# Kernel tuning notes

Hardware: AMD Instinct MI355X
Metric: run time of the kernel (lower is better)

## Reference

```python
import jax, jax.numpy as jnp
import numpy as np

N_USER, N_FOOD, N_ING, N_CAT, N_HAB = 50000, 50000, 50000, 5000, 5000
N_NODES = N_USER + N_FOOD + N_ING + N_CAT + N_HAB  # 160000
E = 600000
R = 8
D = 128  # common_dim == hidden_dim


def _linear(x, W, b):
    # W: (in, out)
    return x @ W + b


def _rgcn_conv(x, src, dst, edge_type, W, root, bias):
    """PyG RGCNConv with aggr='mean': out = x@root + bias + sum_r mean_{r-edges into i}(W_r x_j)."""
    n = x.shape[0]
    out = x @ root + bias
    for r in range(R):  # static small loop over relations
        mask = (edge_type == r)
        h_r = x @ W[r]                          # (N, O)
        msg = h_r[src] * mask[:, None].astype(x.dtype)  # (E, O)
        s = jax.ops.segment_sum(msg, dst, num_segments=n)
        cnt = jax.ops.segment_sum(mask.astype(x.dtype), dst, num_segments=n)
        out = out + s / jnp.maximum(cnt, 1.0)[:, None]
    return out


def setup_inputs() -> dict:
    key = jax.random.key(0)
    ks = jax.random.split(key, 32)
    s = 0.05
    inp = {
        'x_user': jax.random.normal(ks[0], (N_USER, 256), jnp.float32),
        'x_food': jax.random.normal(ks[1], (N_FOOD, 128), jnp.float32),
        'x_ingredient': jax.random.normal(ks[2], (N_ING, 128), jnp.float32),
        'x_category': jax.random.normal(ks[3], (N_CAT, 64), jnp.float32),
        'x_habit': jax.random.normal(ks[4], (N_HAB, 64), jnp.float32),
        'edge_index': jax.random.randint(ks[5], (2, E), 0, N_NODES, jnp.int32),
        'edge_type': jax.random.randint(ks[6], (E,), 0, R, jnp.int32),
        # init linears (in, out)
        'Wu': jax.random.normal(ks[7], (256, D), jnp.float32) * s,
        'bu': jnp.zeros((D,), jnp.float32),
        'Wf': jax.random.normal(ks[8], (128, D), jnp.float32) * s,
        'bf': jnp.zeros((D,), jnp.float32),
        'Wi': jax.random.normal(ks[9], (128, D), jnp.float32) * s,
        'bi': jnp.zeros((D,), jnp.float32),
        'Wc': jax.random.normal(ks[10], (64, D), jnp.float32) * s,
        'bc': jnp.zeros((D,), jnp.float32),
        'Wh': jax.random.normal(ks[11], (64, D), jnp.float32) * s,
        'bh': jnp.zeros((D,), jnp.float32),
        # conv1
        'W1': jax.random.normal(ks[12], (R, D, D), jnp.float32) * s,
        'root1': jax.random.normal(ks[13], (D, D), jnp.float32) * s,
        'bias1': jnp.zeros((D,), jnp.float32),
        # conv2
        'W2': jax.random.normal(ks[14], (R, D, D), jnp.float32) * s,
        'root2': jax.random.normal(ks[15], (D, D), jnp.float32) * s,
        'bias2': jnp.zeros((D,), jnp.float32),
    }
    return inp


def reference(x_user, x_food, x_ingredient, x_category, x_habit,
              edge_index, edge_type,
              Wu, bu, Wf, bf, Wi, bi, Wc, bc, Wh, bh,
              W1, root1, bias1, W2, root2, bias2):
    # per-type input projections then concat in fixed order
    x_all = jnp.concatenate([
        _linear(x_user, Wu, bu),
        _linear(x_food, Wf, bf),
        _linear(x_ingredient, Wi, bi),
        _linear(x_category, Wc, bc),
        _linear(x_habit, Wh, bh),
    ], axis=0)  # (N_NODES, D)
    src, dst = edge_index[0], edge_index[1]
    x = _rgcn_conv(x_all, src, dst, edge_type, W1, root1, bias1)
    x = jax.nn.relu(x)
    # dropout is identity in eval mode
    x = _rgcn_conv(x, src, dst, edge_type, W2, root2, bias2)
    return x
```

## Files before the change

### kernel.cpp

```cpp
#include <hip/hip_runtime.h>

typedef unsigned short ushort_t;
typedef unsigned int uint_t;
typedef __attribute__((ext_vector_type(8))) __bf16 bf16x8;
typedef __attribute__((ext_vector_type(4))) float f32x4;
typedef __attribute__((ext_vector_type(4))) uint_t uint4v;

#define NN 160000
#define DD 128
#define EE 600000
#define RR 8
#define NRR (NN * RR)
#define WTOT 376832

__device__ __forceinline__ ushort_t f2b(float f) {
  uint_t u = __float_as_uint(f);
  u = u + 0x7fffu + ((u >> 16) & 1u);
  return (ushort_t)(u >> 16);
}
__device__ __forceinline__ float b2f(ushort_t u) {
  return __uint_as_float(((uint_t)u) << 16);
}

__device__ __forceinline__ void gload_lds16(const ushort_t* g, ushort_t* l) {
  __builtin_amdgcn_global_load_lds(
      (const __attribute__((address_space(1))) void*)g,
      (__attribute__((address_space(3))) void*)l, 16, 0, 0);
}

struct WSrcs { const float* s[9]; };

__global__ void wconv_all_kernel(WSrcs srcs, ushort_t* __restrict__ wbuf) {
  int i = blockIdx.x * blockDim.x + threadIdx.x;
  if (i >= WTOT) return;
  int m, start, K;
  if      (i < 32768)  { m = 0; start = 0;      K = 256; }
  else if (i < 49152)  { m = 1; start = 32768;  K = 128; }
  else if (i < 65536)  { m = 2; start = 49152;  K = 128; }
  else if (i < 73728)  { m = 3; start = 65536;  K = 64;  }
  else if (i < 81920)  { m = 4; start = 73728;  K = 64;  }
  else if (i < 98304)  { m = 5; start = 81920;  K = 128; }
  else if (i < 114688) { m = 6; start = 98304;  K = 128; }
  else if (i < 245760) { m = 7; start = 114688; K = 128; }
  else                 { m = 8; start = 245760; K = 128; }
  int local = i - start;
  int per = K * 128;
  int mat = local / per, rem = local - mat * per;
  int k = rem >> 7, n = rem & 127;
  ushort_t v = f2b(srcs.s[m][local]);
  if (m < 5) {
    wbuf[start + mat * per + n * K + k] = v;
  } else {
    int kc = k >> 3, kr = k & 7;
    int slot = kc ^ (n & 7);
    wbuf[start + mat * per + n * 128 + slot * 8 + kr] = v;
  }
}

__global__ __launch_bounds__(256, 2) void gemm_proj(
    const float* __restrict__ Ain, const ushort_t* __restrict__ WT,
    const float* __restrict__ bias, ushort_t* __restrict__ Cout, int M, int K) {
  __shared__ ushort_t As[128 * 128];
  __shared__ ushort_t Ws[128 * 128];
  const int tid = threadIdx.x;
  const int bm = blockIdx.x * 128;
  const int wave = tid >> 6, lane = tid & 63;
  const int lr = lane & 15;
  const int lg = lane >> 4;

  f32x4 acc[2][8];
#pragma unroll
  for (int mt = 0; mt < 2; ++mt)
#pragma unroll
    for (int nt = 0; nt < 8; ++nt) acc[mt][nt] = {0.f, 0.f, 0.f, 0.f};

  for (int k0 = 0; k0 < K; k0 += 128) {
#pragma unroll
    for (int it = 0; it < 8; ++it) {
      int row = it * 16 + (tid >> 4);
      int c = tid & 15;
      uint4v val = {0, 0, 0, 0};
      int grow = bm + row, gk = k0 + c * 8;
      if (grow < M && gk < K) {
        const float* ap = Ain + (size_t)grow * K + gk;
        float4 v0 = *(const float4*)ap;
        float4 v1 = *(const float4*)(ap + 4);
        val[0] = (uint_t)f2b(v0.x) | ((uint_t)f2b(v0.y) << 16);
        val[1] = (uint_t)f2b(v0.z) | ((uint_t)f2b(v0.w) << 16);
        val[2] = (uint_t)f2b(v1.x) | ((uint_t)f2b(v1.y) << 16);
        val[3] = (uint_t)f2b(v1.z) | ((uint_t)f2b(v1.w) << 16);
      }
      *(uint4v*)&As[row * 128 + ((c ^ (row & 7)) * 8)] = val;
    }
#pragma unroll
    for (int it = 0; it < 8; ++it) {
      int n = it * 16 + (tid >> 4);
      int c = tid & 15;
      uint4v val = {0, 0, 0, 0};
      int gk = k0 + c * 8;
      if (gk < K)
        val = *(const uint4v*)(WT + (size_t)n * K + gk);
      *(uint4v*)&Ws[n * 128 + ((c ^ (n & 7)) * 8)] = val;
    }
    __syncthreads();
#pragma unroll
    for (int ks = 0; ks < 4; ++ks) {
      int chunk = ks * 4 + lg;
      bf16x8 af[2], bfr[8];
#pragma unroll
      for (int mt = 0; mt < 2; ++mt) {
        int row = wave * 32 + mt * 16 + lr;
        af[mt] = *(const bf16x8*)&As[row * 128 + ((chunk ^ (row & 7)) * 8)];
      }
#pragma unroll
      for (int nt = 0; nt < 8; ++nt) {
        int n = nt * 16 + lr;
        bfr[nt] = *(const bf16x8*)&Ws[n * 128 + ((chunk ^ (n & 7)) * 8)];
      }
#pragma unroll
      for (int mt = 0; mt < 2; ++mt)
#pragma unroll
        for (int nt = 0; nt < 8; ++nt)
          acc[mt][nt] = __builtin_amdgcn_mfma_f32_16x16x32_bf16(
              af[mt], bfr[nt], acc[mt][nt], 0, 0, 0);
    }
    __syncthreads();
  }

  float bv[8];
#pragma unroll
  for (int nt = 0; nt < 8; ++nt) bv[nt] = bias[nt * 16 + lr];

#pragma unroll
  for (int mt = 0; mt < 2; ++mt) {
    int rbase = bm + wave * 32 + mt * 16 + lg * 4;
#pragma unroll
    for (int i = 0; i < 4; ++i) {
      int row = rbase + i;
      if (row >= M) continue;
#pragma unroll
      for (int nt = 0; nt < 8; ++nt)
        Cout[(size_t)row * 128 + nt * 16 + lr] = f2b(acc[mt][nt][i] + bv[nt]);
    }
  }
}

template <bool RELU_BF>
__global__ __launch_bounds__(512, 4) void rgcn_conv(
    const ushort_t* __restrict__ xin, const int* __restrict__ seg_off,
    const int* __restrict__ sorted_src,
    const ushort_t* __restrict__ WrT,
    const ushort_t* __restrict__ rootT,
    const float* __restrict__ bias,
    float* __restrict__ fout, ushort_t* __restrict__ bfout) {
  __shared__ ushort_t As[64 * 128];
  __shared__ ushort_t Ws[128 * 128];
  const int tid = threadIdx.x;
  const int bm = blockIdx.x * 64;
  const int wave = tid >> 6, lane = tid & 63;
  const int wm = wave & 3;
  const int wn = wave >> 2;
  const int lr = lane & 15, lg = lane >> 4;
  const int grp = tid >> 4;
  const int sl = tid & 15;

  f32x4 acc[4];
#pragma unroll
  for (int nt = 0; nt < 4; ++nt) acc[nt] = {0.f, 0.f, 0.f, 0.f};

  int gsv[8][2], gev[8][2];
  int s0v[8][2], s1v[8][2];
  uint4v f0v[8][2], f1v[8][2];
  uint4v rootv[2];

#define BOUNDS(P)                                                         \
  {                                                                       \
    _Pragma("unroll") for (int q = 0; q < 2; ++q) {                       \
      int g = (P) * NN + bm + q * 32 + grp;                               \
      gsv[P][q] = seg_off[g];                                             \
      gev[P][q] = seg_off[g + 1];                                         \
    }                                                                     \
  }

#define SRCS(P)                                                           \
  {                                                                       \
    _Pragma("unroll") for (int q = 0; q < 2; ++q) {                       \
      int a = gsv[P][q];                                                  \
      int c = gev[P][q] - a;                                              \
      int i0 = (a < EE - 1) ? a : (EE - 1);                               \
      int i1 = (c > 1) ? (a + 1) : i0;                                    \
      s0v[P][q] = sorted_src[i0];                                         \
      s1v[P][q] = sorted_src[i1];                                         \
    }                                                                     \
  }

#define FVLOAD(P)                                                         \
  {                                                                       \
    _Pragma("unroll") for (int q = 0; q < 2; ++q) {                       \
      f0v[P][q] = *(const uint4v*)(xin + (size_t)s0v[P][q] * DD + sl * 8);\
      f1v[P][q] = *(const uint4v*)(xin + (size_t)s1v[P][q] * DD + sl * 8);\
    }                                                                     \
  }

#define GLLW(SRC)                                                         \
  {                                                                       \
    const ushort_t* wsrc = (SRC) + (size_t)wave * 2048 + lane * 8;        \
    _Pragma("unroll") for (int i = 0; i < 4; ++i)                         \
      gload_lds16(wsrc + i * 512, &Ws[wave * 2048 + i * 512]);            \
  }

  BOUNDS(0); BOUNDS(1); BOUNDS(2);
  GLLW(WrT);
  SRCS(0); SRCS(1);
  FVLOAD(0);
  __builtin_amdgcn_sched_barrier(0);

#pragma unroll
  for (int p = 0; p < 8; ++p) {
#pragma unroll
    for (int q = 0; q < 2; ++q) {
      int row = q * 32 + grp;
      int a = gsv[p][q];
      int c = gev[p][q] - a;
      uint4v o = {0, 0, 0, 0};
      if (c == 1) {
        o = f0v[p][q];
      } else if (c == 2) {
        uint4v x0 = f0v[p][q], x1 = f1v[p][q];
#pragma unroll
        for (int j = 0; j < 4; ++j) {
          float e0 = (b2f((ushort_t)(x0[j] & 0xffff)) + b2f((ushort_t)(x1[j] & 0xffff))) * 0.5f;
          float e1 = (b2f((ushort_t)(x0[j] >> 16)) + b2f((ushort_t)(x1[j] >> 16))) * 0.5f;
          o[j] = (uint_t)f2b(e0) | ((uint_t)f2b(e1) << 16);
        }
      } else if (c >= 3) {
        uint4v x0 = f0v[p][q], x1 = f1v[p][q];
        float av[8];
#pragma unroll
        for (int j = 0; j < 4; ++j) {
          av[j * 2]     = b2f((ushort_t)(x0[j] & 0xffff)) + b2f((ushort_t)(x1[j] & 0xffff));
          av[j * 2 + 1] = b2f((ushort_t)(x0[j] >> 16)) + b2f((ushort_t)(x1[j] >> 16));
        }
        for (int i = a + 2; i < a + c; ++i) {
          int s = sorted_src[i];
          uint4v v2 = *(const uint4v*)(xin + (size_t)s * DD + sl * 8);
#pragma unroll
          for (int j = 0; j < 4; ++j) {
            av[j * 2]     += b2f((ushort_t)(v2[j] & 0xffff));
            av[j * 2 + 1] += b2f((ushort_t)(v2[j] >> 16));
          }
        }
        float sc = 1.0f / (float)c;
#pragma unroll
        for (int j = 0; j < 4; ++j)
          o[j] = (uint_t)f2b(av[j * 2] * sc) | ((uint_t)f2b(av[j * 2 + 1] * sc) << 16);
      }
      *(uint4v*)&As[row * 128 + ((sl ^ (row & 7)) * 8)] = o;
    }

    __syncthreads();

    if (p < 7) {
      FVLOAD(p + 1);
    } else {
#pragma unroll
      for (int q = 0; q < 2; ++q)
        rootv[q] = *(const uint4v*)(xin + (size_t)(bm + q * 32 + grp) * DD + sl * 8);
    }
    __builtin_amdgcn_sched_barrier(0);

#pragma unroll
    for (int ks = 0; ks < 4; ++ks) {
      int chunk = ks * 4 + lg;
      int arow = wm * 16 + lr;
      bf16x8 af = *(const bf16x8*)&As[arow * 128 + ((chunk ^ (arow & 7)) * 8)];
      bf16x8 bfr[4];
#pragma unroll
      for (int nt = 0; nt < 4; ++nt) {
        int n = (wn * 4 + nt) * 16 + lr;
        bfr[nt] = *(const bf16x8*)&Ws[n * 128 + ((chunk ^ (n & 7)) * 8)];
      }
#pragma unroll
      for (int nt = 0; nt < 4; ++nt)
        acc[nt] = __builtin_amdgcn_mfma_f32_16x16x32_bf16(af, bfr[nt], acc[nt], 0, 0, 0);
    }

    asm volatile("s_waitcnt lgkmcnt(0)" ::: "memory");
    __builtin_amdgcn_s_barrier();
    __builtin_amdgcn_sched_barrier(0);

    if (p < 7) {
      GLLW(WrT + (size_t)(p + 1) * 16384);
    } else {
      GLLW(rootT);
    }
    if (p < 6) { SRCS(p + 2); }
    if (p < 5) { BOUNDS(p + 3); }
    __builtin_amdgcn_sched_barrier(0);
  }

#pragma unroll
  for (int q = 0; q < 2; ++q) {
    int row = q * 32 + grp;
    *(uint4v*)&As[row * 128 + ((sl ^ (row & 7)) * 8)] = rootv[q];
  }
  __syncthreads();
#pragma unroll
  for (int ks = 0; ks < 4; ++ks) {
    int chunk = ks * 4 + lg;
    int arow = wm * 16 + lr;
    bf16x8 af = *(const bf16x8*)&As[arow * 128 + ((chunk ^ (arow & 7)) * 8)];
    bf16x8 bfr[4];
#pragma unroll
    for (int nt = 0; nt < 4; ++nt) {
      int n = (wn * 4 + nt) * 16 + lr;
      bfr[nt] = *(const bf16x8*)&Ws[n * 128 + ((chunk ^ (n & 7)) * 8)];
    }
#pragma unroll
    for (int nt = 0; nt < 4; ++nt)
      acc[nt] = __builtin_amdgcn_mfma_f32_16x16x32_bf16(af, bfr[nt], acc[nt], 0, 0, 0);
  }

  float bv[4];
#pragma unroll
  for (int nt = 0; nt < 4; ++nt) bv[nt] = bias[(wn * 4 + nt) * 16 + lr];

  int rbase = bm + wm * 16 + lg * 4;
#pragma unroll
  for (int i = 0; i < 4; ++i) {
    int row = rbase + i;
#pragma unroll
    for (int nt = 0; nt < 4; ++nt) {
      int col = (wn * 4 + nt) * 16 + lr;
      float v = acc[nt][i] + bv[nt];
      if (RELU_BF)
        bfout[(size_t)row * 128 + col] = f2b(fmaxf(v, 0.f));
      else
        fout[(size_t)row * 128 + col] = v;
    }
  }
#undef BOUNDS
#undef SRCS
#undef FVLOAD
#undef GLLW
}

__global__ void count_kernel(const int* __restrict__ dstv, const int* __restrict__ et,
                             int* __restrict__ cnt, int E) {
  int e = blockIdx.x * blockDim.x + threadIdx.x;
  if (e < E) atomicAdd(&cnt[(size_t)et[e] * NN + dstv[e]], 1);
}

__global__ __launch_bounds__(256) void scan1_kernel(const int* __restrict__ in, int* __restrict__ out,
                                                    int* __restrict__ partials, int n) {
  __shared__ int sums[256];
  int tid = threadIdx.x;
  int base = blockIdx.x * 2048 + tid * 8;
  int v[8];
  int s = 0;
#pragma unroll
  for (int i = 0; i < 8; ++i) {
    int idx = base + i;
    int x = (idx < n) ? in[idx] : 0;
    v[i] = s;
    s += x;
  }
  sums[tid] = s;
  __syncthreads();
  for (int off = 1; off < 256; off <<= 1) {
    int t = (tid >= off) ? sums[tid - off] : 0;
    __syncthreads();
    sums[tid] += t;
    __syncthreads();
  }
  int excl = (tid == 0) ? 0 : sums[tid - 1];
  if (tid == 255) partials[blockIdx.x] = sums[255];
#pragma unroll
  for (int i = 0; i < 8; ++i) {
    int idx = base + i;
    if (idx < n) out[idx] = excl + v[i];
  }
}

__global__ __launch_bounds__(256) void scan2_kernel(int* __restrict__ partials, int nb) {
  __shared__ int sums[256];
  int tid = threadIdx.x;
  int per = (nb + 255) / 256;
  int start = tid * per;
  int s = 0;
  for (int i = 0; i < per; ++i) {
    int idx = start + i;
    if (idx < nb) s += partials[idx];
  }
  sums[tid] = s;
  __syncthreads();
  for (int off = 1; off < 256; off <<= 1) {
    int t = (tid >= off) ? sums[tid - off] : 0;
    __syncthreads();
    sums[tid] += t;
    __syncthreads();
  }
  int excl = (tid == 0) ? 0 : sums[tid - 1];
  for (int i = 0; i < per; ++i) {
    int idx = start + i;
    if (idx < nb) {
      int t = partials[idx];
      partials[idx] = excl;
      excl += t;
    }
  }
}

__global__ void scan3_kernel(int* __restrict__ out, const int* __restrict__ partials, int n) {
  int base = blockIdx.x * 2048 + threadIdx.x * 8;
  int add = partials[blockIdx.x];
#pragma unroll
  for (int i = 0; i < 8; ++i) {
    int idx = base + i;
    if (idx < n) out[idx] += add;
  }
  if (blockIdx.x == 0 && threadIdx.x == 0) out[n] = EE;
}

__global__ void place_kernel(const int* __restrict__ srcv, const int* __restrict__ dstv,
                             const int* __restrict__ et, const int* __restrict__ seg_off,
                             int* __restrict__ cursor, int* __restrict__ sorted_src, int E) {
  int e = blockIdx.x * blockDim.x + threadIdx.x;
  if (e < E) {
    int p = et[e] * NN + dstv[e];
    int slot = seg_off[p] + atomicAdd(&cursor[p], 1);
    sorted_src[slot] = srcv[e];
  }
}

static inline void launch_proj(const float* A, const ushort_t* WT, const float* bias,
                               ushort_t* C, int M, int K, hipStream_t stream) {
  hipLaunchKernelGGL(gemm_proj, dim3((M + 127) / 128), dim3(256), 0, stream,
                     A, WT, bias, C, M, K);
}

extern "C" void kernel_launch(void* const* d_in, const int* in_sizes, int n_in,
                              void* d_out, int out_size, void* d_ws, size_t ws_size,
                              hipStream_t stream) {
  const float* x_user = (const float*)d_in[0];
  const float* x_food = (const float*)d_in[1];
  const float* x_ing  = (const float*)d_in[2];
  const float* x_cat  = (const float*)d_in[3];
  const float* x_hab  = (const float*)d_in[4];
  const int*   eidx   = (const int*)d_in[5];
  const int*   etype  = (const int*)d_in[6];
  const float* Wu = (const float*)d_in[7];
  const float* bu = (const float*)d_in[8];
  const float* Wf = (const float*)d_in[9];
  const float* bfp = (const float*)d_in[10];
  const float* Wi = (const float*)d_in[11];
  const float* bi = (const float*)d_in[12];
  const float* Wc = (const float*)d_in[13];
  const float* bc = (const float*)d_in[14];
  const float* Wh = (const float*)d_in[15];
  const float* bh = (const float*)d_in[16];
  const float* W1    = (const float*)d_in[17];
  const float* root1 = (const float*)d_in[18];
  const float* bias1 = (const float*)d_in[19];
  const float* W2    = (const float*)d_in[20];
  const float* root2 = (const float*)d_in[21];
  const float* bias2 = (const float*)d_in[22];

  const int* src = eidx;
  const int* dst = eidx + EE;

  char* ws = (char*)d_ws;
  ushort_t* xb   = (ushort_t*)(ws);
  ushort_t* xb2  = (ushort_t*)(ws + 40960000);
  int* seg_off   = (int*)(ws + 81920000);
  int* cnt_i     = (int*)(ws + 87040064);
  int* sorted_src= (int*)(ws + 92160064);
  int* pA        = (int*)(ws + 94560064);
  ushort_t* wbuf = (ushort_t*)(ws + 94564160);

  ushort_t* WuT = wbuf;
  ushort_t* WfT = wbuf + 32768;
  ushort_t* WiT = wbuf + 49152;
  ushort_t* WcT = wbuf + 65536;
  ushort_t* WhT = wbuf + 73728;
  ushort_t* r1T = wbuf + 81920;
  ushort_t* r2T = wbuf + 98304;
  ushort_t* W1T = wbuf + 114688;
  ushort_t* W2T = wbuf + 245760;

  float* out = (float*)d_out;

  WSrcs wsrc;
  wsrc.s[0] = Wu; wsrc.s[1] = Wf; wsrc.s[2] = Wi; wsrc.s[3] = Wc; wsrc.s[4] = Wh;
  wsrc.s[5] = root1; wsrc.s[6] = root2; wsrc.s[7] = W1; wsrc.s[8] = W2;
  hipLaunchKernelGGL(wconv_all_kernel, dim3((WTOT + 255) / 256), dim3(256), 0, stream,
                     wsrc, wbuf);

  launch_proj(x_user, WuT, bu, xb + (size_t)0 * DD,      50000, 256, stream);
  launch_proj(x_food, WfT, bfp, xb + (size_t)50000 * DD, 50000, 128, stream);
  launch_proj(x_ing,  WiT, bi, xb + (size_t)100000 * DD, 50000, 128, stream);
  launch_proj(x_cat,  WcT, bc, xb + (size_t)150000 * DD, 5000,  64,  stream);
  launch_proj(x_hab,  WhT, bh, xb + (size_t)155000 * DD, 5000,  64,  stream);

  hipMemsetAsync(cnt_i, 0, (size_t)NRR * 4, stream);
  hipLaunchKernelGGL(count_kernel, dim3((EE + 255) / 256), dim3(256), 0, stream,
                     dst, etype, cnt_i, EE);
  {
    int nb = (NRR + 2047) / 2048;
    hipLaunchKernelGGL(scan1_kernel, dim3(nb), dim3(256), 0, stream, cnt_i, seg_off, pA, NRR);
    hipLaunchKernelGGL(scan2_kernel, dim3(1), dim3(256), 0, stream, pA, nb);
    hipLaunchKernelGGL(scan3_kernel, dim3(nb), dim3(256), 0, stream, seg_off, pA, NRR);
  }
  hipMemsetAsync(cnt_i, 0, (size_t)NRR * 4, stream);
  hipLaunchKernelGGL(place_kernel, dim3((EE + 255) / 256), dim3(256), 0, stream,
                     src, dst, etype, seg_off, cnt_i, sorted_src, EE);

  const dim3 convGrid(NN / 64);

  hipLaunchKernelGGL((rgcn_conv<true>), convGrid, dim3(512), 0, stream,
                     xb, seg_off, sorted_src, W1T, r1T, bias1, (float*)nullptr, xb2);

  hipLaunchKernelGGL((rgcn_conv<false>), convGrid, dim3(512), 0, stream,
                     xb2, seg_off, sorted_src, W2T, r2T, bias2, out, (ushort_t*)nullptr);
}
```

Baseline: 395.2 us.

## Double conv row tile to 128 and remap waves to 2x4 MFMA layout

Each rgcn_conv block now handles 128 destination rows instead of 64. Each wave computes a 64x32 output sub-tile (4 row tiles by 2 column tiles) rather than 16x64, so every per-relation weight tile staged into LDS feeds twice as many rows and the global weight traffic is halved. The cost is a larger As buffer (64 KB of LDS with Ws) and twice the per-thread prefetch register arrays, which will likely lower occupancy below the launch-bounds target and may cause spills. The grid also shrinks to 1250 blocks, which fills the CUs less evenly.

Measured after the change: 406.5 us. +2.9%, slower.

```diff
diff --git a/kernel.cpp b/kernel.cpp
--- a/kernel.cpp
+++ b/kernel.cpp
@@ -153,29 +153,31 @@
     const ushort_t* __restrict__ rootT,
     const float* __restrict__ bias,
     float* __restrict__ fout, ushort_t* __restrict__ bfout) {
-  __shared__ ushort_t As[64 * 128];
+  __shared__ ushort_t As[128 * 128];
   __shared__ ushort_t Ws[128 * 128];
   const int tid = threadIdx.x;
-  const int bm = blockIdx.x * 64;
+  const int bm = blockIdx.x * 128;
   const int wave = tid >> 6, lane = tid & 63;
-  const int wm = wave & 3;
-  const int wn = wave >> 2;
+  const int wm = wave & 1;
+  const int wn = wave >> 1;
   const int lr = lane & 15, lg = lane >> 4;
   const int grp = tid >> 4;
   const int sl = tid & 15;
 
-  f32x4 acc[4];
-#pragma unroll
-  for (int nt = 0; nt < 4; ++nt) acc[nt] = {0.f, 0.f, 0.f, 0.f};
-
-  int gsv[8][2], gev[8][2];
-  int s0v[8][2], s1v[8][2];
-  uint4v f0v[8][2], f1v[8][2];
-  uint4v rootv[2];
+  f32x4 acc[4][2];
+#pragma unroll
+  for (int rt = 0; rt < 4; ++rt)
+#pragma unroll
+    for (int ct = 0; ct < 2; ++ct) acc[rt][ct] = {0.f, 0.f, 0.f, 0.f};
+
+  int gsv[8][4], gev[8][4];
+  int s0v[8][4], s1v[8][4];
+  uint4v f0v[8][4], f1v[8][4];
+  uint4v rootv[4];
 
 #define BOUNDS(P)                                                         \
   {                                                                       \
-    _Pragma("unroll") for (int q = 0; q < 2; ++q) {                       \
+    _Pragma("unroll") for (int q = 0; q < 4; ++q) {                       \
       int g = (P) * NN + bm + q * 32 + grp;                               \
       gsv[P][q] = seg_off[g];                                             \
       gev[P][q] = seg_off[g + 1];                                         \
@@ -184,7 +186,7 @@
 
 #define SRCS(P)                                                           \
   {                                                                       \
-    _Pragma("unroll") for (int q = 0; q < 2; ++q) {                       \
+    _Pragma("unroll") for (int q = 0; q < 4; ++q) {                       \
       int a = gsv[P][q];                                                  \
       int c = gev[P][q] - a;                                              \
       int i0 = (a < EE - 1) ? a : (EE - 1);                               \
@@ -196,7 +198,7 @@
 
 #define FVLOAD(P)                                                         \
   {                                                                       \
-    _Pragma("unroll") for (int q = 0; q < 2; ++q) {                       \
+    _Pragma("unroll") for (int q = 0; q < 4; ++q) {                       \
       f0v[P][q] = *(const uint4v*)(xin + (size_t)s0v[P][q] * DD + sl * 8);\
       f1v[P][q] = *(const uint4v*)(xin + (size_t)s1v[P][q] * DD + sl * 8);\
     }                                                                     \
@@ -218,7 +220,7 @@
 #pragma unroll
   for (int p = 0; p < 8; ++p) {
 #pragma unroll
-    for (int q = 0; q < 2; ++q) {
+    for (int q = 0; q < 4; ++q) {
       int row = q * 32 + grp;
       int a = gsv[p][q];
       int c = gev[p][q] - a;
@@ -264,7 +266,7 @@
       FVLOAD(p + 1);
     } else {
 #pragma unroll
-      for (int q = 0; q < 2; ++q)
+      for (int q = 0; q < 4; ++q)
         rootv[q] = *(const uint4v*)(xin + (size_t)(bm + q * 32 + grp) * DD + sl * 8);
     }
     __builtin_amdgcn_sched_barrier(0);
@@ -272,17 +274,23 @@
 #pragma unroll
     for (int ks = 0; ks < 4; ++ks) {
       int chunk = ks * 4 + lg;
-      int arow = wm * 16 + lr;
-      bf16x8 af = *(const bf16x8*)&As[arow * 128 + ((chunk ^ (arow & 7)) * 8)];
-      bf16x8 bfr[4];
-#pragma unroll
-      for (int nt = 0; nt < 4; ++nt) {
-        int n = (wn * 4 + nt) * 16 + lr;
-        bfr[nt] = *(const bf16x8*)&Ws[n * 128 + ((chunk ^ (n & 7)) * 8)];
-      }
-#pragma unroll
-      for (int nt = 0; nt < 4; ++nt)
-        acc[nt] = __builtin_amdgcn_mfma_f32_16x16x32_bf16(af, bfr[nt], acc[nt], 0, 0, 0);
+      bf16x8 af[4], bfr[2];
+#pragma unroll
+      for (int rt = 0; rt < 4; ++rt) {
+        int arow = wm * 64 + rt * 16 + lr;
+        af[rt] = *(const bf16x8*)&As[arow * 128 + ((chunk ^ (arow & 7)) * 8)];
+      }
+#pragma unroll
+      for (int ct = 0; ct < 2; ++ct) {
+        int n = wn * 32 + ct * 16 + lr;
+        bfr[ct] = *(const bf16x8*)&Ws[n * 128 + ((chunk ^ (n & 7)) * 8)];
+      }
+#pragma unroll
+      for (int rt = 0; rt < 4; ++rt)
+#pragma unroll
+        for (int ct = 0; ct < 2; ++ct)
+          acc[rt][ct] = __builtin_amdgcn_mfma_f32_16x16x32_bf16(
+              af[rt], bfr[ct], acc[rt][ct], 0, 0, 0);
     }
 
     asm volatile("s_waitcnt lgkmcnt(0)" ::: "memory");
@@ -300,7 +308,7 @@
   }
 
 #pragma unroll
-  for (int q = 0; q < 2; ++q) {
+  for (int q = 0; q < 4; ++q) {
     int row = q * 32 + grp;
     *(uint4v*)&As[row * 128 + ((sl ^ (row & 7)) * 8)] = rootv[q];
   }
@@ -308,35 +316,44 @@
 #pragma unroll
   for (int ks = 0; ks < 4; ++ks) {
     int chunk = ks * 4 + lg;
-    int arow = wm * 16 + lr;
-    bf16x8 af = *(const bf16x8*)&As[arow * 128 + ((chunk ^ (arow & 7)) * 8)];
-    bf16x8 bfr[4];
-#pragma unroll
-    for (int nt = 0; nt < 4; ++nt) {
-      int n = (wn * 4 + nt) * 16 + lr;
-      bfr[nt] = *(const bf16x8*)&Ws[n * 128 + ((chunk ^ (n & 7)) * 8)];
-    }
-#pragma unroll
-    for (int nt = 0; nt < 4; ++nt)
-      acc[nt] = __builtin_amdgcn_mfma_f32_16x16x32_bf16(af, bfr[nt], acc[nt], 0, 0, 0);
-  }
-
-  float bv[4];
-#pragma unroll
-  for (int nt = 0; nt < 4; ++nt) bv[nt] = bias[(wn * 4 + nt) * 16 + lr];
-
-  int rbase = bm + wm * 16 + lg * 4;
-#pragma unroll
-  for (int i = 0; i < 4; ++i) {
-    int row = rbase + i;
-#pragma unroll
-    for (int nt = 0; nt < 4; ++nt) {
-      int col = (wn * 4 + nt) * 16 + lr;
-      float v = acc[nt][i] + bv[nt];
-      if (RELU_BF)
-        bfout[(size_t)row * 128 + col] = f2b(fmaxf(v, 0.f));
-      else
-        fout[(size_t)row * 128 + col] = v;
+    bf16x8 af[4], bfr[2];
+#pragma unroll
+    for (int rt = 0; rt < 4; ++rt) {
+      int arow = wm * 64 + rt * 16 + lr;
+      af[rt] = *(const bf16x8*)&As[arow * 128 + ((chunk ^ (arow & 7)) * 8)];
+    }
+#pragma unroll
+    for (int ct = 0; ct < 2; ++ct) {
+      int n = wn * 32 + ct * 16 + lr;
+      bfr[ct] = *(const bf16x8*)&Ws[n * 128 + ((chunk ^ (n & 7)) * 8)];
+    }
+#pragma unroll
+    for (int rt = 0; rt < 4; ++rt)
+#pragma unroll
+      for (int ct = 0; ct < 2; ++ct)
+        acc[rt][ct] = __builtin_amdgcn_mfma_f32_16x16x32_bf16(
+            af[rt], bfr[ct], acc[rt][ct], 0, 0, 0);
+  }
+
+  float bv[2];
+#pragma unroll
+  for (int ct = 0; ct < 2; ++ct) bv[ct] = bias[wn * 32 + ct * 16 + lr];
+
+#pragma unroll
+  for (int rt = 0; rt < 4; ++rt) {
+    int rbase = bm + wm * 64 + rt * 16 + lg * 4;
+#pragma unroll
+    for (int i = 0; i < 4; ++i) {
+      int row = rbase + i;
+#pragma unroll
+      for (int ct = 0; ct < 2; ++ct) {
+        int col = wn * 32 + ct * 16 + lr;
+        float v = acc[rt][ct][i] + bv[ct];
+        if (RELU_BF)
+          bfout[(size_t)row * 128 + col] = f2b(fmaxf(v, 0.f));
+        else
+          fout[(size_t)row * 128 + col] = v;
+      }
     }
   }
 #undef BOUNDS
@@ -515,7 +532,7 @@
   hipLaunchKernelGGL(place_kernel, dim3((EE + 255) / 256), dim3(256), 0, stream,
                      src, dst, etype, seg_off, cnt_i, sorted_src, EE);
 
-  const dim3 convGrid(NN / 64);
+  const dim3 convGrid(NN / 128);
 
   hipLaunchKernelGGL((rgcn_conv<true>), convGrid, dim3(512), 0, stream,
                      xb, seg_off, sorted_src, W1T, r1T, bias1, (float*)nullptr, xb2);
```
